# Kernel tuning notes

Hardware: AMD Instinct MI355X
Metric: run time of the kernel (lower is better)

The kernel has to match this reference:

```python
import jax, jax.numpy as jnp
import numpy as np

N, LC, LQ, D = 16, 2048, 256, 256  # D = 2 * LSTM_HIDDEN_DIM


def setup_inputs() -> dict:
    key = jax.random.key(0)
    k1, k2, k3 = jax.random.split(key, 3)
    emb_context = jax.random.normal(k1, (N, LC, D), dtype=jnp.float32)
    emb_query = jax.random.normal(k2, (N, LQ, D), dtype=jnp.float32)
    # Linear(6H=3D, 1, bias=False) weight, flattened to (3D,)
    W = jax.random.normal(k3, (3 * D,), dtype=jnp.float32) / np.sqrt(3 * D)
    return {"emb_context": emb_context, "emb_query": emb_query, "W": W}


def reference(emb_context, emb_query, W):
    d = emb_context.shape[-1]
    # Algebraic decomposition of the expand+cat+linear similarity score:
    # S[n,i,j] = c_i . w_c + q_j . w_q + sum_d c_i[d]*q_j[d]*w_m[d]
    w_c, w_q, w_m = W[:d], W[d:2 * d], W[2 * d:]
    S = (
        jnp.einsum('ncd,d->nc', emb_context, w_c)[:, :, None]
        + jnp.einsum('nqd,d->nq', emb_query, w_q)[:, None, :]
        + jnp.einsum('ncd,nqd->ncq', emb_context * w_m, emb_query)
    )  # (N, Lc, Lq)
    # context-to-query attention
    c2q_attn = jnp.einsum('ncq,nqd->ncd', jax.nn.softmax(S, axis=-1), emb_query)
    # query-to-context attention (max over query dim, softmax over context dim)
    b = jax.nn.softmax(jnp.max(S, axis=2), axis=-1)  # (N, Lc)
    q2c_attn = jnp.einsum('nc,ncd->nd', b, emb_context)[:, None, :]  # (N, 1, D), broadcasts over Lc
    G = jnp.concatenate(
        [emb_context, c2q_attn, emb_context * c2q_attn, emb_context * q2c_attn],
        axis=2,
    )  # (N, Lc, 4D) == (N, Lc, 8*LSTM_HIDDEN_DIM)
    return G
```

## Files before the change

kernel.cpp:

```cpp
#include <hip/hip_runtime.h>
#include <math.h>

#define BN 16
#define LC 2048
#define LQ 256
#define DD 256
#define BM 64

typedef _Float16 half8 __attribute__((ext_vector_type(8)));
typedef float f32x16 __attribute__((ext_vector_type(16)));

__device__ __forceinline__ float waveReduceSum(float v) {
#pragma unroll
    for (int o = 32; o > 0; o >>= 1) v += __shfl_xor(v, o, 64);
    return v;
}
__device__ __forceinline__ float waveReduceMax(float v) {
#pragma unroll
    for (int o = 32; o > 0; o >>= 1) v = fmaxf(v, __shfl_xor(v, o, 64));
    return v;
}

__global__ __launch_bounds__(256) void k_prep(const float* __restrict__ q,
                                              const float* __restrict__ W,
                                              _Float16* __restrict__ Qh,
                                              _Float16* __restrict__ QTh,
                                              float* __restrict__ cq) {
    __shared__ float tile[32][257];
    const int n = blockIdx.y;
    const int q0 = blockIdx.x * 32;
    const int t = threadIdx.x;

#pragma unroll
    for (int i = 0; i < 32; ++i) {
        const float v = q[((size_t)(n * LQ + q0 + i)) * DD + t];
        Qh[((size_t)(n * LQ + q0 + i)) * DD + t] = (_Float16)v;
        tile[i][t] = v;
    }
    __syncthreads();

    {
        const int row = t >> 3, sub = t & 7;
        float s = 0.f;
#pragma unroll
        for (int j = 0; j < 32; ++j)
            s = fmaf(tile[row][sub * 32 + j], W[DD + sub * 32 + j], s);
        s += __shfl_xor(s, 1, 64);
        s += __shfl_xor(s, 2, 64);
        s += __shfl_xor(s, 4, 64);
        if (sub == 0) cq[n * LQ + q0 + row] = s;
    }

    const int tx = t & 31, ty = t >> 5;
#pragma unroll
    for (int db = 0; db < 8; ++db) {
#pragma unroll
        for (int i = 0; i < 4; ++i) {
            const int d = db * 32 + ty + 8 * i;
            QTh[((size_t)(n * DD + d)) * LQ + q0 + tx] = (_Float16)tile[tx][d];
        }
    }
}

__global__ __launch_bounds__(256) void k_main(const float* __restrict__ ctx,
                                              const _Float16* __restrict__ Qh,
                                              const _Float16* __restrict__ QTh,
                                              const float* __restrict__ cq,
                                              const float* __restrict__ W,
                                              float* __restrict__ out,
                                              float* __restrict__ pq,
                                              float* __restrict__ KS) {
    __shared__ _Float16 Abuf[BM * 256];
    __shared__ _Float16 Bbuf[256 * 64];
    __shared__ float rowterm[BM];
    __shared__ float m_lds[BM];
    __shared__ float linv_lds[BM];
    __shared__ float eexp[BM];
    __shared__ float redmax[4][BM];
    __shared__ float redsum[4][BM];

    const int t = threadIdx.x;
    const int lane = t & 63, wid = t >> 6;
    const int l31 = lane & 31, lh = lane >> 5;
    const int blk = blockIdx.x;
    const int n = blk >> 5;
    const int blk32 = blk & 31;
    const int c0 = blk32 * BM;

    const _Float16* Qhn = Qh + (size_t)n * LQ * DD;
    const _Float16* QThn = QTh + (size_t)n * DD * LQ;

    auto stageB = [&](int kc, const _Float16* src) {
        const int g = t & 7;
        const int rb = t >> 3;
#pragma unroll
        for (int i = 0; i < 8; ++i) {
            const int r = rb + 32 * i;
            const half8 v = *(const half8*)(src + (size_t)r * 256 + kc * 64 + g * 8);
            *(half8*)((char*)Bbuf + r * 128 + ((g * 16) ^ ((r & 7) << 4))) = v;
        }
    };

    stageB(0, Qhn);

    {
        const int g = t & 31;
        const int r0 = t >> 5;
        float wmv[8], wcv[8];
#pragma unroll
        for (int j = 0; j < 8; ++j) {
            wmv[j] = W[2 * DD + g * 8 + j];
            wcv[j] = W[g * 8 + j];
        }
#pragma unroll
        for (int i = 0; i < 8; ++i) {
            const int r = r0 + 8 * i;
            const float* srcr = ctx + ((size_t)(n * LC + c0 + r)) * DD + g * 8;
            const float4 aa = *(const float4*)srcr;
            const float4 bb = *(const float4*)(srcr + 4);
            const float vals[8] = {aa.x, aa.y, aa.z, aa.w, bb.x, bb.y, bb.z, bb.w};
            half8 cmv;
            float rt = 0.f;
#pragma unroll
            for (int j = 0; j < 8; ++j) {
                cmv[j] = (_Float16)(vals[j] * wmv[j]);
                rt = fmaf(vals[j], wcv[j], rt);
            }
            *(half8*)((char*)Abuf + r * 512 + ((g * 16) ^ ((r & 7) << 4))) = cmv;
#pragma unroll
            for (int o = 16; o > 0; o >>= 1) rt += __shfl_xor(rt, o, 64);
            if (g == 0) rowterm[r] = rt;
        }
    }
    __syncthreads();

    f32x16 acc[2][2] = {};
    for (int kc = 0; kc < 4; ++kc) {
        if (kc > 0) {
            __syncthreads();
            stageB(kc, Qhn);
            __syncthreads();
        }
#pragma unroll
        for (int kk = 0; kk < 4; ++kk) {
            half8 af[2], bf[2];
#pragma unroll
            for (int mt = 0; mt < 2; ++mt) {
                const int row = 32 * mt + l31;
                const int kb = kc * 128 + 32 * kk + 16 * lh;
                af[mt] = *(const half8*)((const char*)Abuf + row * 512 + (kb ^ ((row & 7) << 4)));
            }
#pragma unroll
            for (int nt = 0; nt < 2; ++nt) {
                const int row = 64 * wid + 32 * nt + l31;
                const int kb = 32 * kk + 16 * lh;
                bf[nt] = *(const half8*)((const char*)Bbuf + row * 128 + (kb ^ ((row & 7) << 4)));
            }
#pragma unroll
            for (int mt = 0; mt < 2; ++mt)
#pragma unroll
                for (int nt = 0; nt < 2; ++nt)
                    acc[mt][nt] = __builtin_amdgcn_mfma_f32_32x32x16_f16(af[mt], bf[nt], acc[mt][nt], 0, 0, 0);
        }
    }
    __syncthreads();

    stageB(0, QThn);

    float cqv[2];
    cqv[0] = cq[n * LQ + 64 * wid + l31];
    cqv[1] = cq[n * LQ + 64 * wid + 32 + l31];

#pragma unroll
    for (int mt = 0; mt < 2; ++mt) {
#pragma unroll
        for (int r = 0; r < 16; ++r) {
            const int rl = 32 * mt + (r & 3) + 8 * (r >> 2) + 4 * lh;
            const float rterm = rowterm[rl];
            const float v0 = acc[mt][0][r] + rterm + cqv[0];
            const float v1 = acc[mt][1][r] + rterm + cqv[1];
            acc[mt][0][r] = v0;
            acc[mt][1][r] = v1;
            float mx = fmaxf(v0, v1);
#pragma unroll
            for (int o = 16; o > 0; o >>= 1) mx = fmaxf(mx, __shfl_xor(mx, o, 64));
            if (l31 == 0) redmax[wid][rl] = mx;
        }
    }
    __syncthreads();
    if (t < BM)
        m_lds[t] = fmaxf(fmaxf(redmax[0][t], redmax[1][t]), fmaxf(redmax[2][t], redmax[3][t]));
    __syncthreads();

    if (t < BM) {
        const float mv = m_lds[t];
        const float kb = waveReduceMax(mv);
        const float e = __expf(mv - kb);
        eexp[t] = e;
        const float sb = waveReduceSum(e);
        if (t == 0) {
            KS[(n * 32 + blk32) * 2 + 0] = kb;
            KS[(n * 32 + blk32) * 2 + 1] = sb;
        }
    }

#pragma unroll
    for (int mt = 0; mt < 2; ++mt) {
#pragma unroll
        for (int r = 0; r < 16; ++r) {
            const int rl = 32 * mt + (r & 3) + 8 * (r >> 2) + 4 * lh;
            const float mrow = m_lds[rl];
            const float p0 = __expf(acc[mt][0][r] - mrow);
            const float p1 = __expf(acc[mt][1][r] - mrow);
            const int q0 = 64 * wid + l31, q1 = q0 + 32;
            *((_Float16*)((char*)Abuf + rl * 512 + ((q0 * 2) ^ ((rl & 7) << 4)))) = (_Float16)p0;
            *((_Float16*)((char*)Abuf + rl * 512 + ((q1 * 2) ^ ((rl & 7) << 4)))) = (_Float16)p1;
            float sm = p0 + p1;
#pragma unroll
            for (int o = 16; o > 0; o >>= 1) sm += __shfl_xor(sm, o, 64);
            if (l31 == 0) redsum[wid][rl] = sm;
        }
    }
    __syncthreads();
    if (t < BM) {
        const float s4 = redsum[0][t] + redsum[1][t] + redsum[2][t] + redsum[3][t];
        linv_lds[t] = 1.0f / s4;
    }
    __syncthreads();

    f32x16 acc2[2][2] = {};
    for (int kc = 0; kc < 4; ++kc) {
        if (kc > 0) {
            __syncthreads();
            stageB(kc, QThn);
            __syncthreads();
        }
#pragma unroll
        for (int kk = 0; kk < 4; ++kk) {
            half8 af[2], bf[2];
#pragma unroll
            for (int mt = 0; mt < 2; ++mt) {
                const int row = 32 * mt + l31;
                const int kb = kc * 128 + 32 * kk + 16 * lh;
                af[mt] = *(const half8*)((const char*)Abuf + row * 512 + (kb ^ ((row & 7) << 4)));
            }
#pragma unroll
            for (int nt = 0; nt < 2; ++nt) {
                const int row = 64 * wid + 32 * nt + l31;
                const int kb = 32 * kk + 16 * lh;
                bf[nt] = *(const half8*)((const char*)Bbuf + row * 128 + (kb ^ ((row & 7) << 4)));
            }
#pragma unroll
            for (int mt = 0; mt < 2; ++mt)
#pragma unroll
                for (int nt = 0; nt < 2; ++nt)
                    acc2[mt][nt] = __builtin_amdgcn_mfma_f32_32x32x16_f16(af[mt], bf[nt], acc2[mt][nt], 0, 0, 0);
        }
    }

    float pqa[2] = {0.f, 0.f};
#pragma unroll
    for (int mt = 0; mt < 2; ++mt) {
#pragma unroll
        for (int nt = 0; nt < 2; ++nt) {
            const int col = 64 * wid + 32 * nt + l31;
#pragma unroll
            for (int r = 0; r < 16; ++r) {
                const int rl = 32 * mt + (r & 3) + 8 * (r >> 2) + 4 * lh;
                const size_t gc = (size_t)(n * LC + c0 + rl);
                const float li = linv_lds[rl];
                const float ctxv = ctx[gc * DD + col];
                const float ov = acc2[mt][nt][r] * li;
                const size_t ob = gc * 1024 + col;
                out[ob] = ctxv;
                out[ob + 256] = ov;
                out[ob + 512] = ctxv * ov;
                pqa[nt] = fmaf(eexp[rl], ctxv, pqa[nt]);
            }
        }
    }
#pragma unroll
    for (int nt = 0; nt < 2; ++nt) {
        pqa[nt] += __shfl_xor(pqa[nt], 32, 64);
        if (lh == 0) {
            const int col = 64 * wid + 32 * nt + l31;
            pq[((size_t)(n * 32 + blk32)) * 256 + col] = pqa[nt];
        }
    }
}

__global__ __launch_bounds__(256) void k_tail(const float* __restrict__ ctx,
                                              const float* __restrict__ pq,
                                              const float* __restrict__ KS,
                                              float* __restrict__ out) {
    const int blk = blockIdx.x;
    const int n = blk >> 5;
    const int c0 = (blk & 31) * BM;
    const int t = threadIdx.x;

    float bmax = -1e30f;
#pragma unroll
    for (int b = 0; b < 32; ++b) bmax = fmaxf(bmax, KS[(n * 32 + b) * 2]);
    float Z = 0.f;
    float acc = 0.f;
#pragma unroll
    for (int b = 0; b < 32; ++b) {
        const float w = __expf(KS[(n * 32 + b) * 2] - bmax);
        Z = fmaf(w, KS[(n * 32 + b) * 2 + 1], Z);
        acc = fmaf(w, pq[((size_t)(n * 32 + b)) * 256 + t], acc);
    }
    const float q2cd = acc / Z;

#pragma unroll 4
    for (int r = 0; r < BM; ++r) {
        const size_t gc = (size_t)(n * LC + c0 + r);
        out[gc * 1024 + 768 + t] = ctx[gc * DD + t] * q2cd;
    }
}

extern "C" void kernel_launch(void* const* d_in, const int* in_sizes, int n_in,
                              void* d_out, int out_size, void* d_ws, size_t ws_size,
                              hipStream_t stream) {
    const float* ctx = (const float*)d_in[0];
    const float* q = (const float*)d_in[1];
    const float* W = (const float*)d_in[2];
    float* out = (float*)d_out;

    _Float16* Qh = (_Float16*)d_ws;
    _Float16* QTh = Qh + (size_t)BN * LQ * DD;
    float* fws = (float*)(QTh + (size_t)BN * DD * LQ);
    float* cq = fws;
    float* pq = cq + BN * LQ;
    float* KS = pq + BN * 32 * 256;

    k_prep<<<dim3(LQ / 32, BN), 256, 0, stream>>>(q, W, Qh, QTh, cq);
    k_main<<<BN * LC / BM, 256, 0, stream>>>(ctx, Qh, QTh, cq, W, out, pq, KS);
    k_tail<<<BN * LC / BM, 256, 0, stream>>>(ctx, pq, KS, out);
}
```

Before: 82.38 us.

## Double-buffer Q tiles via direct global-to-LDS loads with 128-row, 512-thread blocks

Each k_main block now covers 128 context rows with 8 waves in a 2x4 wave grid, so every staged Q chunk is reused by twice as many rows. Q/QT chunks are staged with global_load_lds into a double-buffered LDS tile, and the next chunk is prefetched while the current one is multiplied, which cuts one barrier per chunk and overlaps loads with MFMA. The cost is doubled LDS for the B buffer and larger blocks, giving half as many blocks and possibly lower occupancy. The KS and pq partials keep a 64-row granularity, so k_tail is unchanged apart from its constants.

```diff
diff --git a/kernel.cpp b/kernel.cpp
--- a/kernel.cpp
+++ b/kernel.cpp
@@ -5,10 +5,16 @@
 #define LC 2048
 #define LQ 256
 #define DD 256
-#define BM 64
+#define BM 128
+#define NT 512
 
 typedef _Float16 half8 __attribute__((ext_vector_type(8)));
 typedef float f32x16 __attribute__((ext_vector_type(16)));
+
+typedef const __attribute__((address_space(1))) void* gas_p;
+typedef __attribute__((address_space(3))) void* lds_p;
+#define GLOAD_LDS16(gp, lp) \
+    __builtin_amdgcn_global_load_lds((gas_p)(gp), (lds_p)(lp), 16, 0, 0)
 
 __device__ __forceinline__ float waveReduceSum(float v) {
 #pragma unroll
@@ -62,16 +68,16 @@
     }
 }
 
-__global__ __launch_bounds__(256) void k_main(const float* __restrict__ ctx,
-                                              const _Float16* __restrict__ Qh,
-                                              const _Float16* __restrict__ QTh,
-                                              const float* __restrict__ cq,
-                                              const float* __restrict__ W,
-                                              float* __restrict__ out,
-                                              float* __restrict__ pq,
-                                              float* __restrict__ KS) {
+__global__ __launch_bounds__(NT) void k_main(const float* __restrict__ ctx,
+                                             const _Float16* __restrict__ Qh,
+                                             const _Float16* __restrict__ QTh,
+                                             const float* __restrict__ cq,
+                                             const float* __restrict__ W,
+                                             float* __restrict__ out,
+                                             float* __restrict__ pq,
+                                             float* __restrict__ KS) {
     __shared__ _Float16 Abuf[BM * 256];
-    __shared__ _Float16 Bbuf[256 * 64];
+    __shared__ _Float16 Bbuf[2][256 * 64];
     __shared__ float rowterm[BM];
     __shared__ float m_lds[BM];
     __shared__ float linv_lds[BM];
@@ -82,26 +88,51 @@
     const int t = threadIdx.x;
     const int lane = t & 63, wid = t >> 6;
     const int l31 = lane & 31, lh = lane >> 5;
+    const int wr = wid >> 2, wc = wid & 3;
     const int blk = blockIdx.x;
-    const int n = blk >> 5;
-    const int blk32 = blk & 31;
-    const int c0 = blk32 * BM;
+    const int n = blk >> 4;
+    const int blk16 = blk & 15;
+    const int c0 = blk16 * BM;
 
     const _Float16* Qhn = Qh + (size_t)n * LQ * DD;
     const _Float16* QThn = QTh + (size_t)n * DD * LQ;
 
-    auto stageB = [&](int kc, const _Float16* src) {
-        const int g = t & 7;
-        const int rb = t >> 3;
-#pragma unroll
-        for (int i = 0; i < 8; ++i) {
-            const int r = rb + 32 * i;
-            const half8 v = *(const half8*)(src + (size_t)r * 256 + kc * 64 + g * 8);
-            *(half8*)((char*)Bbuf + r * 128 + ((g * 16) ^ ((r & 7) << 4))) = v;
+    auto stageB = [&](int kc, const _Float16* src, int buf) {
+#pragma unroll
+        for (int j = 0; j < 4; ++j) {
+            const int r = wid * 32 + j * 8 + (lane >> 3);
+            const int gs = (lane & 7) ^ (r & 7);
+            const _Float16* gp = src + (size_t)r * 256 + kc * 64 + gs * 8;
+            _Float16* lp = &Bbuf[buf][(wid * 32 + j * 8) * 64];
+            GLOAD_LDS16(gp, lp);
         }
     };
 
-    stageB(0, Qhn);
+    auto gemmChunk = [&](f32x16 (&acc)[2][2], int kcA, int buf) {
+#pragma unroll
+        for (int kk = 0; kk < 4; ++kk) {
+            half8 af[2], bf[2];
+#pragma unroll
+            for (int mt = 0; mt < 2; ++mt) {
+                const int row = 64 * wr + 32 * mt + l31;
+                const int kb = kcA * 128 + 32 * kk + 16 * lh;
+                af[mt] = *(const half8*)((const char*)Abuf + row * 512 + (kb ^ ((row & 7) << 4)));
+            }
+#pragma unroll
+            for (int nt = 0; nt < 2; ++nt) {
+                const int row = 64 * wc + 32 * nt + l31;
+                const int kb = 32 * kk + 16 * lh;
+                bf[nt] = *(const half8*)((const char*)Bbuf[buf] + row * 128 + (kb ^ ((row & 7) << 4)));
+            }
+#pragma unroll
+            for (int mt = 0; mt < 2; ++mt)
+#pragma unroll
+                for (int nt = 0; nt < 2; ++nt)
+                    acc[mt][nt] = __builtin_amdgcn_mfma_f32_32x32x16_f16(af[mt], bf[nt], acc[mt][nt], 0, 0, 0);
+        }
+    };
+
+    stageB(0, Qhn, 0);
 
     {
         const int g = t & 31;
@@ -114,7 +145,7 @@
         }
 #pragma unroll
         for (int i = 0; i < 8; ++i) {
-            const int r = r0 + 8 * i;
+            const int r = r0 + 16 * i;
             const float* srcr = ctx + ((size_t)(n * LC + c0 + r)) * DD + g * 8;
             const float4 aa = *(const float4*)srcr;
             const float4 bb = *(const float4*)(srcr + 4);
@@ -135,47 +166,24 @@
     __syncthreads();
 
     f32x16 acc[2][2] = {};
+#pragma unroll
     for (int kc = 0; kc < 4; ++kc) {
-        if (kc > 0) {
-            __syncthreads();
-            stageB(kc, Qhn);
-            __syncthreads();
-        }
-#pragma unroll
-        for (int kk = 0; kk < 4; ++kk) {
-            half8 af[2], bf[2];
-#pragma unroll
-            for (int mt = 0; mt < 2; ++mt) {
-                const int row = 32 * mt + l31;
-                const int kb = kc * 128 + 32 * kk + 16 * lh;
-                af[mt] = *(const half8*)((const char*)Abuf + row * 512 + (kb ^ ((row & 7) << 4)));
-            }
-#pragma unroll
-            for (int nt = 0; nt < 2; ++nt) {
-                const int row = 64 * wid + 32 * nt + l31;
-                const int kb = 32 * kk + 16 * lh;
-                bf[nt] = *(const half8*)((const char*)Bbuf + row * 128 + (kb ^ ((row & 7) << 4)));
-            }
-#pragma unroll
-            for (int mt = 0; mt < 2; ++mt)
-#pragma unroll
-                for (int nt = 0; nt < 2; ++nt)
-                    acc[mt][nt] = __builtin_amdgcn_mfma_f32_32x32x16_f16(af[mt], bf[nt], acc[mt][nt], 0, 0, 0);
-        }
-    }
-    __syncthreads();
-
-    stageB(0, QThn);
+        if (kc) __syncthreads();
+        if (kc < 3) stageB(kc + 1, Qhn, (kc + 1) & 1);
+        else stageB(0, QThn, 0);
+        gemmChunk(acc, kc, kc & 1);
+    }
+    __syncthreads();
 
     float cqv[2];
-    cqv[0] = cq[n * LQ + 64 * wid + l31];
-    cqv[1] = cq[n * LQ + 64 * wid + 32 + l31];
+    cqv[0] = cq[n * LQ + 64 * wc + l31];
+    cqv[1] = cq[n * LQ + 64 * wc + 32 + l31];
 
 #pragma unroll
     for (int mt = 0; mt < 2; ++mt) {
 #pragma unroll
         for (int r = 0; r < 16; ++r) {
-            const int rl = 32 * mt + (r & 3) + 8 * (r >> 2) + 4 * lh;
+            const int rl = 64 * wr + 32 * mt + (r & 3) + 8 * (r >> 2) + 4 * lh;
             const float rterm = rowterm[rl];
             const float v0 = acc[mt][0][r] + rterm + cqv[0];
             const float v1 = acc[mt][1][r] + rterm + cqv[1];
@@ -184,7 +192,7 @@
             float mx = fmaxf(v0, v1);
 #pragma unroll
             for (int o = 16; o > 0; o >>= 1) mx = fmaxf(mx, __shfl_xor(mx, o, 64));
-            if (l31 == 0) redmax[wid][rl] = mx;
+            if (l31 == 0) redmax[wc][rl] = mx;
         }
     }
     __syncthreads();
@@ -198,9 +206,9 @@
         const float e = __expf(mv - kb);
         eexp[t] = e;
         const float sb = waveReduceSum(e);
-        if (t == 0) {
-            KS[(n * 32 + blk32) * 2 + 0] = kb;
-            KS[(n * 32 + blk32) * 2 + 1] = sb;
+        if (lane == 0) {
+            KS[(n * 32 + blk16 * 2 + (t >> 6)) * 2 + 0] = kb;
+            KS[(n * 32 + blk16 * 2 + (t >> 6)) * 2 + 1] = sb;
         }
     }
 
@@ -208,54 +216,30 @@
     for (int mt = 0; mt < 2; ++mt) {
 #pragma unroll
         for (int r = 0; r < 16; ++r) {
-            const int rl = 32 * mt + (r & 3) + 8 * (r >> 2) + 4 * lh;
+            const int rl = 64 * wr + 32 * mt + (r & 3) + 8 * (r >> 2) + 4 * lh;
             const float mrow = m_lds[rl];
             const float p0 = __expf(acc[mt][0][r] - mrow);
             const float p1 = __expf(acc[mt][1][r] - mrow);
-            const int q0 = 64 * wid + l31, q1 = q0 + 32;
+            const int q0 = 64 * wc + l31, q1 = q0 + 32;
             *((_Float16*)((char*)Abuf + rl * 512 + ((q0 * 2) ^ ((rl & 7) << 4)))) = (_Float16)p0;
             *((_Float16*)((char*)Abuf + rl * 512 + ((q1 * 2) ^ ((rl & 7) << 4)))) = (_Float16)p1;
             float sm = p0 + p1;
 #pragma unroll
             for (int o = 16; o > 0; o >>= 1) sm += __shfl_xor(sm, o, 64);
-            if (l31 == 0) redsum[wid][rl] = sm;
-        }
-    }
-    __syncthreads();
-    if (t < BM) {
-        const float s4 = redsum[0][t] + redsum[1][t] + redsum[2][t] + redsum[3][t];
-        linv_lds[t] = 1.0f / s4;
-    }
+            if (l31 == 0) redsum[wc][rl] = sm;
+        }
+    }
+    __syncthreads();
+    if (t < BM)
+        linv_lds[t] = 1.0f / (redsum[0][t] + redsum[1][t] + redsum[2][t] + redsum[3][t]);
     __syncthreads();
 
     f32x16 acc2[2][2] = {};
+#pragma unroll
     for (int kc = 0; kc < 4; ++kc) {
-        if (kc > 0) {
-            __syncthreads();
-            stageB(kc, QThn);
-            __syncthreads();
-        }
-#pragma unroll
-        for (int kk = 0; kk < 4; ++kk) {
-            half8 af[2], bf[2];
-#pragma unroll
-            for (int mt = 0; mt < 2; ++mt) {
-                const int row = 32 * mt + l31;
-                const int kb = kc * 128 + 32 * kk + 16 * lh;
-                af[mt] = *(const half8*)((const char*)Abuf + row * 512 + (kb ^ ((row & 7) << 4)));
-            }
-#pragma unroll
-            for (int nt = 0; nt < 2; ++nt) {
-                const int row = 64 * wid + 32 * nt + l31;
-                const int kb = 32 * kk + 16 * lh;
-                bf[nt] = *(const half8*)((const char*)Bbuf + row * 128 + (kb ^ ((row & 7) << 4)));
-            }
-#pragma unroll
-            for (int mt = 0; mt < 2; ++mt)
-#pragma unroll
-                for (int nt = 0; nt < 2; ++nt)
-                    acc2[mt][nt] = __builtin_amdgcn_mfma_f32_32x32x16_f16(af[mt], bf[nt], acc2[mt][nt], 0, 0, 0);
-        }
+        if (kc) __syncthreads();
+        if (kc < 3) stageB(kc + 1, QThn, (kc + 1) & 1);
+        gemmChunk(acc2, kc, kc & 1);
     }
 
     float pqa[2] = {0.f, 0.f};
@@ -263,10 +247,10 @@
     for (int mt = 0; mt < 2; ++mt) {
 #pragma unroll
         for (int nt = 0; nt < 2; ++nt) {
-            const int col = 64 * wid + 32 * nt + l31;
+            const int col = 64 * wc + 32 * nt + l31;
 #pragma unroll
             for (int r = 0; r < 16; ++r) {
-                const int rl = 32 * mt + (r & 3) + 8 * (r >> 2) + 4 * lh;
+                const int rl = 64 * wr + 32 * mt + (r & 3) + 8 * (r >> 2) + 4 * lh;
                 const size_t gc = (size_t)(n * LC + c0 + rl);
                 const float li = linv_lds[rl];
                 const float ctxv = ctx[gc * DD + col];
@@ -283,8 +267,8 @@
     for (int nt = 0; nt < 2; ++nt) {
         pqa[nt] += __shfl_xor(pqa[nt], 32, 64);
         if (lh == 0) {
-            const int col = 64 * wid + 32 * nt + l31;
-            pq[((size_t)(n * 32 + blk32)) * 256 + col] = pqa[nt];
+            const int col = 64 * wc + 32 * nt + l31;
+            pq[((size_t)(n * 32 + blk16 * 2 + wr)) * 256 + col] = pqa[nt];
         }
     }
 }
@@ -295,7 +279,7 @@
                                               float* __restrict__ out) {
     const int blk = blockIdx.x;
     const int n = blk >> 5;
-    const int c0 = (blk & 31) * BM;
+    const int c0 = (blk & 31) * 64;
     const int t = threadIdx.x;
 
     float bmax = -1e30f;
@@ -312,7 +296,7 @@
     const float q2cd = acc / Z;
 
 #pragma unroll 4
-    for (int r = 0; r < BM; ++r) {
+    for (int r = 0; r < 64; ++r) {
         const size_t gc = (size_t)(n * LC + c0 + r);
         out[gc * 1024 + 768 + t] = ctx[gc * DD + t] * q2cd;
     }
@@ -334,6 +318,6 @@
     float* KS = pq + BN * 32 * 256;
 
     k_prep<<<dim3(LQ / 32, BN), 256, 0, stream>>>(q, W, Qh, QTh, cq);
-    k_main<<<BN * LC / BM, 256, 0, stream>>>(ctx, Qh, QTh, cq, W, out, pq, KS);
-    k_tail<<<BN * LC / BM, 256, 0, stream>>>(ctx, pq, KS, out);
-}
+    k_main<<<BN * LC / BM, NT, 0, stream>>>(ctx, Qh, QTh, cq, W, out, pq, KS);
+    k_tail<<<BN * LC / 64, 256, 0, stream>>>(ctx, pq, KS, out);
+}
```

Result: faster. 70.64 us (-14.3%).
